# Kernel tuning notes

Measured on AMD Instinct MI355X. Metric: run time of the kernel, lower is better.

Reference implementation:

```python
import jax, jax.numpy as jnp
import numpy as np

B = 65536
N_WORKER, N_PROJECT, EMB = 1807, 2490, 10
STATE_DIM = 2 * EMB          # 20
HIDDEN = 2 * STATE_DIM       # 40
ACTION_DIM = EMB             # 10


def setup_inputs() -> dict:
    key = jax.random.key(0)
    ks = jax.random.split(key, 8)
    worker_ids = jax.random.randint(ks[0], (B,), 0, N_WORKER)
    project_ids = jax.random.randint(ks[1], (B,), 0, N_PROJECT)
    worker_emb = jax.random.normal(ks[2], (N_WORKER, EMB), dtype=jnp.float32)
    project_emb = jax.random.normal(ks[3], (N_PROJECT, EMB), dtype=jnp.float32)
    W1 = jax.random.normal(ks[4], (HIDDEN, STATE_DIM), dtype=jnp.float32) / np.sqrt(STATE_DIM)
    b1 = jnp.zeros((HIDDEN,), dtype=jnp.float32)
    W2 = jax.random.normal(ks[5], (ACTION_DIM, HIDDEN), dtype=jnp.float32) / np.sqrt(HIDDEN)
    b2 = jnp.zeros((ACTION_DIM,), dtype=jnp.float32)
    return {"worker_ids": worker_ids, "project_ids": project_ids,
            "worker_emb": worker_emb, "project_emb": project_emb,
            "W1": W1, "b1": b1, "W2": W2, "b2": b2}


def reference(worker_ids, project_ids, worker_emb, project_emb, W1, b1, W2, b2):
    we = worker_emb[worker_ids]              # [B, 10]
    pe = project_emb[project_ids]            # [B, 10]
    x = jnp.concatenate([we, pe], axis=-1)   # [B, 20]
    h = jax.nn.relu(x @ W1.T + b1)           # [B, 40]
    the_weights = (h @ W2.T + b2)[:, None, :]  # [B, 1, 10]
    # original loop rebuilds rows 1..2489 of the project table -> single slice
    table = project_emb[1:N_PROJECT]         # [2489, 10]
    p = jnp.einsum('bqd,nd->bqn', the_weights, table)  # [B, 1, 2489]
    argmax = jnp.argmax(p, axis=2)           # [B, 1]
    return argmax + 1
```

## Files before the change

kernel.cpp:

```cpp
#include <hip/hip_runtime.h>
#include <float.h>

using v2f = __attribute__((ext_vector_type(2))) float;
using v4f = __attribute__((ext_vector_type(4))) float;

#define EMB 10
#define STATE 20
#define HIDDEN 40
#define NPROJ 2490
#define WAVES 16
#define ITEMS 128

__global__ __launch_bounds__(256, 4) void mlp_kernel(
    const int* __restrict__ wid, const int* __restrict__ pid,
    const float* __restrict__ wemb, const float* __restrict__ pemb,
    const float* __restrict__ W1, const float* __restrict__ b1,
    const float* __restrict__ W2, const float* __restrict__ b2,
    float* __restrict__ ws)
{
    const int b = blockIdx.x * 256 + threadIdx.x;

    const int wi = wid[b];
    const int pi = pid[b];
    const float* __restrict__ wr = wemb + wi * EMB;
    const float* __restrict__ pr = pemb + pi * EMB;
    v2f x2[STATE / 2];
    #pragma unroll
    for (int k = 0; k < EMB / 2; ++k) x2[k] = *(const v2f*)(wr + 2 * k);
    #pragma unroll
    for (int k = 0; k < EMB / 2; ++k) x2[EMB / 2 + k] = *(const v2f*)(pr + 2 * k);

    float hb[HIDDEN];
    #pragma unroll 4
    for (int j = 0; j < HIDDEN; ++j) {
        const v2f* w1r = (const v2f*)(W1 + j * STATE);
        v2f a = w1r[0] * x2[0];
        #pragma unroll
        for (int k = 1; k < STATE / 2; ++k) a += w1r[k] * x2[k];
        hb[j] = fmaxf(a.x + a.y + b1[j], 0.0f);
    }
    v2f h2[HIDDEN / 2];
    #pragma unroll
    for (int k = 0; k < HIDDEN / 2; ++k) h2[k] = (v2f){hb[2 * k], hb[2 * k + 1]};

    v2f* wout = (v2f*)(ws + b * EMB);
    #pragma unroll
    for (int d = 0; d < EMB; d += 2) {
        const v2f* w2r0 = (const v2f*)(W2 + d * HIDDEN);
        const v2f* w2r1 = (const v2f*)(W2 + (d + 1) * HIDDEN);
        v2f a0 = w2r0[0] * h2[0];
        v2f a1 = w2r1[0] * h2[0];
        #pragma unroll
        for (int k = 1; k < HIDDEN / 2; ++k) { a0 += w2r0[k] * h2[k]; a1 += w2r1[k] * h2[k]; }
        wout[d / 2] = (v2f){a0.x + a0.y + b2[d], a1.x + a1.y + b2[d + 1]};
    }
}

__device__ __forceinline__ void score_pair2(const v4f* __restrict__ tp, int p,
                                            const v2f wv[2][5],
                                            float best[2], int bidx[2]) {
    v4f a0 = tp[0], a1 = tp[1], a2 = tp[2], a3 = tp[3], a4 = tp[4];
    #pragma unroll
    for (int g = 0; g < 2; ++g) {
        v2f c0 = wv[g][0] * a0.lo;
        c0 += wv[g][1] * a0.hi; c0 += wv[g][2] * a1.lo;
        c0 += wv[g][3] * a1.hi; c0 += wv[g][4] * a2.lo;
        float s0 = c0.x + c0.y;
        v2f c1 = wv[g][0] * a2.hi;
        c1 += wv[g][1] * a3.lo; c1 += wv[g][2] * a3.hi;
        c1 += wv[g][3] * a4.lo; c1 += wv[g][4] * a4.hi;
        float s1 = c1.x + c1.y;
        float sp = s0; int ip = 2 * p;
        if (s1 > sp) { sp = s1; ip = 2 * p + 1; }
        if (sp > best[g]) { best[g] = sp; bidx[g] = ip; }
    }
}

template <int P0, int P1>
__device__ __forceinline__ void scan_range(const v4f* __restrict__ tbl4,
                                           const v2f wv[2][5],
                                           float best[2], int bidx[2]) {
    const v4f* tp = tbl4 + P0 * 5;
    #pragma unroll 4
    for (int p = P0; p < P1; ++p, tp += 5) score_pair2(tp, p, wv, best, bidx);
}

__global__ __launch_bounds__(1024, 8) void scan_kernel(
    const float* __restrict__ pemb, const float* __restrict__ ws,
    int* __restrict__ out)
{
    __shared__ float sb[WAVES][ITEMS];
    __shared__ int   si[WAVES][ITEMS];

    const int tid  = threadIdx.x;
    const int lane = tid & 63;
    const int wave = tid >> 6;
    const int itemBase = blockIdx.x * ITEMS;

    const v4f* __restrict__ tbl4 =
        (const v4f*)__builtin_assume_aligned(pemb, 16);

    v2f wv[2][5];
    #pragma unroll
    for (int g = 0; g < 2; ++g) {
        const v2f* src = (const v2f*)(ws + (itemBase + g * 64 + lane) * EMB);
        #pragma unroll
        for (int k = 0; k < 5; ++k) wv[g][k] = src[k];
    }

    float best[2];
    int   bidx[2];
    #pragma unroll
    for (int g = 0; g < 2; ++g) { best[g] = -FLT_MAX; bidx[g] = 1; }

    if (wave == 0) {
        v2f c0v = *(const v2f*)(pemb + 10);
        v4f c1v = *(const v4f*)(pemb + 12);
        v4f c2v = *(const v4f*)(pemb + 16);
        #pragma unroll
        for (int g = 0; g < 2; ++g) {
            v2f a = wv[g][0] * c0v;
            a += wv[g][1] * c1v.lo; a += wv[g][2] * c1v.hi;
            a += wv[g][3] * c2v.lo; a += wv[g][4] * c2v.hi;
            best[g] = a.x + a.y; bidx[g] = 1;
        }
    }

    switch (wave) {
        case  0: scan_range<   1,   79>(tbl4, wv, best, bidx); break;
        case  1: scan_range<  79,  157>(tbl4, wv, best, bidx); break;
        case  2: scan_range< 157,  235>(tbl4, wv, best, bidx); break;
        case  3: scan_range< 235,  313>(tbl4, wv, best, bidx); break;
        case  4: scan_range< 313,  391>(tbl4, wv, best, bidx); break;
        case  5: scan_range< 391,  469>(tbl4, wv, best, bidx); break;
        case  6: scan_range< 469,  547>(tbl4, wv, best, bidx); break;
        case  7: scan_range< 547,  625>(tbl4, wv, best, bidx); break;
        case  8: scan_range< 625,  703>(tbl4, wv, best, bidx); break;
        case  9: scan_range< 703,  781>(tbl4, wv, best, bidx); break;
        case 10: scan_range< 781,  859>(tbl4, wv, best, bidx); break;
        case 11: scan_range< 859,  937>(tbl4, wv, best, bidx); break;
        case 12: scan_range< 937, 1014>(tbl4, wv, best, bidx); break;
        case 13: scan_range<1014, 1091>(tbl4, wv, best, bidx); break;
        case 14: scan_range<1091, 1168>(tbl4, wv, best, bidx); break;
        case 15: scan_range<1168, 1245>(tbl4, wv, best, bidx); break;
    }

    #pragma unroll
    for (int g = 0; g < 2; ++g) {
        sb[wave][g * 64 + lane] = best[g];
        si[wave][g * 64 + lane] = bidx[g];
    }
    __syncthreads();

    if (tid < ITEMS) {
        float bb = sb[0][tid];
        int   bi = si[0][tid];
        #pragma unroll
        for (int w = 1; w < WAVES; ++w) {
            float v  = sb[w][tid];
            int   vi = si[w][tid];
            if (v > bb) { bb = v; bi = vi; }
        }
        out[itemBase + tid] = bi;
    }
}

__device__ __forceinline__ void score_pair2_rt(const v4f* __restrict__ tp, int p,
                                               const v2f wv[2][5],
                                               float best[2], int bidx[2]) {
    score_pair2(tp, p, wv, best, bidx);
}

__global__ __launch_bounds__(1024, 8) void actor_kernel(
    const int* __restrict__ wid, const int* __restrict__ pid,
    const float* __restrict__ wemb, const float* __restrict__ pemb,
    const float* __restrict__ W1, const float* __restrict__ b1,
    const float* __restrict__ W2, const float* __restrict__ b2,
    int* __restrict__ out)
{
    __shared__ v2f   sw[ITEMS][5];
    __shared__ float sb[WAVES][ITEMS];
    __shared__ int   si[WAVES][ITEMS];

    const int tid  = threadIdx.x;
    const int lane = tid & 63;
    const int wave = tid >> 6;
    const int itemBase = blockIdx.x * ITEMS;

    const v4f* __restrict__ tbl4 =
        (const v4f*)__builtin_assume_aligned(pemb, 16);

    if (wave < ITEMS / 64) {
        const int b = itemBase + wave * 64 + lane;
        const int wi = wid[b];
        const int pi = pid[b];
        const float* __restrict__ wr = wemb + wi * EMB;
        const float* __restrict__ pr = pemb + pi * EMB;
        v2f x2[STATE / 2];
        #pragma unroll
        for (int k = 0; k < EMB / 2; ++k) x2[k] = *(const v2f*)(wr + 2 * k);
        #pragma unroll
        for (int k = 0; k < EMB / 2; ++k) x2[EMB / 2 + k] = *(const v2f*)(pr + 2 * k);

        float hb[HIDDEN];
        #pragma unroll 4
        for (int j = 0; j < HIDDEN; ++j) {
            const v2f* w1r = (const v2f*)(W1 + j * STATE);
            v2f a = w1r[0] * x2[0];
            #pragma unroll
            for (int k = 1; k < STATE / 2; ++k) a += w1r[k] * x2[k];
            hb[j] = fmaxf(a.x + a.y + b1[j], 0.0f);
        }
        v2f h2[HIDDEN / 2];
        #pragma unroll
        for (int k = 0; k < HIDDEN / 2; ++k) h2[k] = (v2f){hb[2 * k], hb[2 * k + 1]};

        #pragma unroll
        for (int d = 0; d < EMB; d += 2) {
            const v2f* w2r0 = (const v2f*)(W2 + d * HIDDEN);
            const v2f* w2r1 = (const v2f*)(W2 + (d + 1) * HIDDEN);
            v2f a0 = w2r0[0] * h2[0];
            v2f a1 = w2r1[0] * h2[0];
            #pragma unroll
            for (int k = 1; k < HIDDEN / 2; ++k) { a0 += w2r0[k] * h2[k]; a1 += w2r1[k] * h2[k]; }
            sw[wave * 64 + lane][d / 2] = (v2f){a0.x + a0.y + b2[d], a1.x + a1.y + b2[d + 1]};
        }
    }
    __syncthreads();

    v2f wv[2][5];
    #pragma unroll
    for (int g = 0; g < 2; ++g) {
        #pragma unroll
        for (int k = 0; k < 5; ++k) wv[g][k] = sw[g * 64 + lane][k];
    }

    float best[2];
    int   bidx[2];
    #pragma unroll
    for (int g = 0; g < 2; ++g) { best[g] = -FLT_MAX; bidx[g] = 1; }

    if (wave == 0) {
        v2f c0v = *(const v2f*)(pemb + 10);
        v4f c1v = *(const v4f*)(pemb + 12);
        v4f c2v = *(const v4f*)(pemb + 16);
        #pragma unroll
        for (int g = 0; g < 2; ++g) {
            v2f a = wv[g][0] * c0v;
            a += wv[g][1] * c1v.lo; a += wv[g][2] * c1v.hi;
            a += wv[g][3] * c2v.lo; a += wv[g][4] * c2v.hi;
            best[g] = a.x + a.y; bidx[g] = 1;
        }
    }

    int start = (wave < 12) ? (1 + 78 * wave) : (937 + 77 * (wave - 12));
    int cnt   = (wave < 12) ? 78 : 77;
    start = __builtin_amdgcn_readfirstlane(start);
    cnt   = __builtin_amdgcn_readfirstlane(cnt);

    const v4f* tp = tbl4 + start * 5;
    #pragma unroll 4
    for (int i = 0; i < cnt; ++i, tp += 5)
        score_pair2_rt(tp, start + i, wv, best, bidx);

    #pragma unroll
    for (int g = 0; g < 2; ++g) {
        sb[wave][g * 64 + lane] = best[g];
        si[wave][g * 64 + lane] = bidx[g];
    }
    __syncthreads();

    if (tid < ITEMS) {
        float bb = sb[0][tid];
        int   bi = si[0][tid];
        #pragma unroll
        for (int w = 1; w < WAVES; ++w) {
            float v  = sb[w][tid];
            int   vi = si[w][tid];
            if (v > bb) { bb = v; bi = vi; }
        }
        out[itemBase + tid] = bi;
    }
}

extern "C" void kernel_launch(void* const* d_in, const int* in_sizes, int n_in,
                              void* d_out, int out_size, void* d_ws, size_t ws_size,
                              hipStream_t stream) {
    const int*   wid  = (const int*)  d_in[0];
    const int*   pid  = (const int*)  d_in[1];
    const float* wemb = (const float*)d_in[2];
    const float* pemb = (const float*)d_in[3];
    const float* W1   = (const float*)d_in[4];
    const float* b1   = (const float*)d_in[5];
    const float* W2   = (const float*)d_in[6];
    const float* b2   = (const float*)d_in[7];
    int* out = (int*)d_out;

    const int B = in_sizes[0];
    const size_t ws_needed = (size_t)B * EMB * sizeof(float);

    if (d_ws != nullptr && ws_size >= ws_needed) {
        float* ws = (float*)d_ws;
        mlp_kernel<<<B / 256, 256, 0, stream>>>(wid, pid, wemb, pemb, W1, b1, W2, b2, ws);
        scan_kernel<<<B / ITEMS, 1024, 0, stream>>>(pemb, ws, out);
    } else {
        actor_kernel<<<B / ITEMS, 1024, 0, stream>>>(wid, pid, wemb, pemb, W1, b1, W2, b2, out);
    }
}
```

Before: 131.4 us.

## Split table scan into two LDS-staged halves with separate combine kernel

Replaces the single scan kernel with a split version. Each group of 128 items is handled by two 512-thread blocks, and each block copies half of the project table into LDS and scans it there with compile-time wave ranges. A third small kernel merges the two partial argmax results. The aim is to serve table reads from LDS instead of global/L1 and to raise block-level parallelism, at the cost of an extra launch, extra workspace traffic, and about 50KB of LDS per block, which limits occupancy.

```diff
diff --git a/kernel.cpp b/kernel.cpp
--- a/kernel.cpp
+++ b/kernel.cpp
@@ -10,6 +10,10 @@
 #define NPROJ 2490
 #define WAVES 16
 #define ITEMS 128
+
+#define HALF_PAIRS 622
+#define HALF_FLOATS (HALF_PAIRS * 20)
+#define HALF_V4 (HALF_FLOATS / 4)
 
 __global__ __launch_bounds__(256, 4) void mlp_kernel(
     const int* __restrict__ wid, const int* __restrict__ pid,
@@ -54,6 +58,126 @@
         for (int k = 1; k < HIDDEN / 2; ++k) { a0 += w2r0[k] * h2[k]; a1 += w2r1[k] * h2[k]; }
         wout[d / 2] = (v2f){a0.x + a0.y + b2[d], a1.x + a1.y + b2[d + 1]};
     }
+}
+
+template <int Q0, int Q1>
+__device__ __forceinline__ void scan_lds_range(const v4f* lt4, int p2base,
+                                               const v2f wv[2][5],
+                                               float best[2], int bidx[2]) {
+    #pragma unroll 4
+    for (int q = Q0; q < Q1; ++q) {
+        const v4f* tq = lt4 + q * 5;
+        v4f a0 = tq[0], a1 = tq[1], a2 = tq[2], a3 = tq[3], a4 = tq[4];
+        #pragma unroll
+        for (int g = 0; g < 2; ++g) {
+            v2f c0 = wv[g][0] * a0.lo;
+            c0 += wv[g][1] * a0.hi; c0 += wv[g][2] * a1.lo;
+            c0 += wv[g][3] * a1.hi; c0 += wv[g][4] * a2.lo;
+            float s0 = c0.x + c0.y;
+            v2f c1 = wv[g][0] * a2.hi;
+            c1 += wv[g][1] * a3.lo; c1 += wv[g][2] * a3.hi;
+            c1 += wv[g][3] * a4.lo; c1 += wv[g][4] * a4.hi;
+            float s1 = c1.x + c1.y;
+            float sp = s0; int ip = p2base + 2 * q;
+            if (s1 > sp) { sp = s1; ip = p2base + 2 * q + 1; }
+            if (sp > best[g]) { best[g] = sp; bidx[g] = ip; }
+        }
+    }
+}
+
+__global__ __launch_bounds__(512, 4) void scan_split_kernel(
+    const float* __restrict__ pemb, const float* __restrict__ wsW,
+    float* __restrict__ wsF, int* __restrict__ wsI)
+{
+    __shared__ float lt[HALF_FLOATS];
+    __shared__ float sb[8][ITEMS];
+    __shared__ int   si[8][ITEMS];
+
+    const int tid   = threadIdx.x;
+    const int lane  = tid & 63;
+    const int wave  = tid >> 6;
+    const int group = blockIdx.x >> 1;
+    const int half  = blockIdx.x & 1;
+    const int itemBase = group * ITEMS;
+
+    v2f wv[2][5];
+    #pragma unroll
+    for (int g = 0; g < 2; ++g) {
+        const v2f* src = (const v2f*)(wsW + (itemBase + g * 64 + lane) * EMB);
+        #pragma unroll
+        for (int k = 0; k < 5; ++k) wv[g][k] = src[k];
+    }
+
+    const v4f* src4 = (const v4f*)(pemb + 20 + half * HALF_FLOATS);
+    v4f* lt4w = (v4f*)lt;
+    for (int j = tid; j < HALF_V4; j += 512) lt4w[j] = src4[j];
+    __syncthreads();
+
+    float best[2];
+    int   bidx[2];
+    #pragma unroll
+    for (int g = 0; g < 2; ++g) { best[g] = -FLT_MAX; bidx[g] = 1; }
+
+    const int p2base = 2 * (1 + HALF_PAIRS * half);
+
+    if (half == 0 && wave == 0) {
+        v2f c0v = *(const v2f*)(pemb + 10);
+        v4f c1v = *(const v4f*)(pemb + 12);
+        v4f c2v = *(const v4f*)(pemb + 16);
+        #pragma unroll
+        for (int g = 0; g < 2; ++g) {
+            v2f a = wv[g][0] * c0v;
+            a += wv[g][1] * c1v.lo; a += wv[g][2] * c1v.hi;
+            a += wv[g][3] * c2v.lo; a += wv[g][4] * c2v.hi;
+            best[g] = a.x + a.y; bidx[g] = 1;
+        }
+    }
+
+    const v4f* lt4 = (const v4f*)lt;
+    switch (wave) {
+        case 0: scan_lds_range<  0,  78>(lt4, p2base, wv, best, bidx); break;
+        case 1: scan_lds_range< 78, 156>(lt4, p2base, wv, best, bidx); break;
+        case 2: scan_lds_range<156, 234>(lt4, p2base, wv, best, bidx); break;
+        case 3: scan_lds_range<234, 312>(lt4, p2base, wv, best, bidx); break;
+        case 4: scan_lds_range<312, 390>(lt4, p2base, wv, best, bidx); break;
+        case 5: scan_lds_range<390, 468>(lt4, p2base, wv, best, bidx); break;
+        case 6: scan_lds_range<468, 545>(lt4, p2base, wv, best, bidx); break;
+        case 7: scan_lds_range<545, 622>(lt4, p2base, wv, best, bidx); break;
+    }
+
+    #pragma unroll
+    for (int g = 0; g < 2; ++g) {
+        sb[wave][g * 64 + lane] = best[g];
+        si[wave][g * 64 + lane] = bidx[g];
+    }
+    __syncthreads();
+
+    if (tid < ITEMS) {
+        float bb = sb[0][tid];
+        int   bi = si[0][tid];
+        #pragma unroll
+        for (int w = 1; w < 8; ++w) {
+            float v  = sb[w][tid];
+            int   vi = si[w][tid];
+            if (v > bb) { bb = v; bi = vi; }
+        }
+        wsF[group * 256 + half * ITEMS + tid] = bb;
+        wsI[group * 256 + half * ITEMS + tid] = bi;
+    }
+}
+
+__global__ __launch_bounds__(256, 8) void combine_kernel(
+    const float* __restrict__ wsF, const int* __restrict__ wsI,
+    int* __restrict__ out)
+{
+    const int i = blockIdx.x * 256 + threadIdx.x;
+    const int g = i >> 7;
+    const int l = i & 127;
+    const float a = wsF[g * 256 + l];
+    const int  ai = wsI[g * 256 + l];
+    const float bv = wsF[g * 256 + 128 + l];
+    const int  bi = wsI[g * 256 + 128 + l];
+    out[i] = (bv > a) ? bi : ai;
 }
 
 __device__ __forceinline__ void score_pair2(const v4f* __restrict__ tp, int p,
@@ -165,12 +289,6 @@
     }
 }
 
-__device__ __forceinline__ void score_pair2_rt(const v4f* __restrict__ tp, int p,
-                                               const v2f wv[2][5],
-                                               float best[2], int bidx[2]) {
-    score_pair2(tp, p, wv, best, bidx);
-}
-
 __global__ __launch_bounds__(1024, 8) void actor_kernel(
     const int* __restrict__ wid, const int* __restrict__ pid,
     const float* __restrict__ wemb, const float* __restrict__ pemb,
@@ -261,7 +379,7 @@
     const v4f* tp = tbl4 + start * 5;
     #pragma unroll 4
     for (int i = 0; i < cnt; ++i, tp += 5)
-        score_pair2_rt(tp, start + i, wv, best, bidx);
+        score_pair2(tp, start + i, wv, best, bidx);
 
     #pragma unroll
     for (int g = 0; g < 2; ++g) {
@@ -297,9 +415,20 @@
     int* out = (int*)d_out;
 
     const int B = in_sizes[0];
-    const size_t ws_needed = (size_t)B * EMB * sizeof(float);
-
-    if (d_ws != nullptr && ws_size >= ws_needed) {
+    const int nGroups = B / ITEMS;
+
+    const size_t wsW_bytes = (size_t)B * EMB * sizeof(float);
+    const size_t wsF_bytes = (size_t)nGroups * 256 * sizeof(float);
+    const size_t wsI_bytes = (size_t)nGroups * 256 * sizeof(int);
+
+    if (d_ws != nullptr && ws_size >= wsW_bytes + wsF_bytes + wsI_bytes) {
+        float* wsW = (float*)d_ws;
+        float* wsF = (float*)((char*)d_ws + wsW_bytes);
+        int*   wsI = (int*)  ((char*)d_ws + wsW_bytes + wsF_bytes);
+        mlp_kernel<<<B / 256, 256, 0, stream>>>(wid, pid, wemb, pemb, W1, b1, W2, b2, wsW);
+        scan_split_kernel<<<nGroups * 2, 512, 0, stream>>>(pemb, wsW, wsF, wsI);
+        combine_kernel<<<B / 256, 256, 0, stream>>>(wsF, wsI, out);
+    } else if (d_ws != nullptr && ws_size >= wsW_bytes) {
         float* ws = (float*)d_ws;
         mlp_kernel<<<B / 256, 256, 0, stream>>>(wid, pid, wemb, pemb, W1, b1, W2, b2, ws);
         scan_kernel<<<B / ITEMS, 1024, 0, stream>>>(pemb, ws, out);
```

Result: no change. 133.7 us (+1.8%).
